# Kernel optimization log

Measured on AMD Instinct MI355X. Metric: run time of the kernel, lower is better.

Reference implementation:

```python
import jax, jax.numpy as jnp
import numpy as np

N, M, D = 256, 1024, 512


def setup_inputs() -> dict:
    key = jax.random.key(0)
    ks = jax.random.split(key, 12)
    s = 1.0 / np.sqrt(D)
    return {
        "q": jax.random.normal(ks[0], (N, D), jnp.float32),
        "k": jax.random.normal(ks[1], (M, D), jnp.float32),
        "v": jax.random.normal(ks[2], (M, D), jnp.float32),
        "mask": jax.random.randint(ks[3], (N, M), 0, 2, jnp.int32),
        "WQ": jax.random.normal(ks[4], (D, D), jnp.float32) * s,
        "bQ": jax.random.normal(ks[5], (D,), jnp.float32) * s,
        "WK": jax.random.normal(ks[6], (D, D), jnp.float32) * s,
        "bK": jax.random.normal(ks[7], (D,), jnp.float32) * s,
        "WV": jax.random.normal(ks[8], (D, D), jnp.float32) * s,
        "bV": jax.random.normal(ks[9], (D,), jnp.float32) * s,
        "Ww": jax.random.normal(ks[10], (1, D), jnp.float32) * s,
        "bw": jax.random.normal(ks[11], (1,), jnp.float32) * s,
    }


def reference(q, k, v, mask, WQ, bQ, WK, bK, WV, bV, Ww, bw):
    # Linear projections (torch Linear: x @ W.T + b)
    qp = q @ WQ.T + bQ            # [N, D]
    kp = k @ WK.T + bK            # [M, D]
    vp = v @ WV.T + bV            # [M, D]
    # Additive (Bahdanau) scores: tanh(q_n + k_m) . w  -> [N, M]
    t = jnp.tanh(qp[:, None, :] + kp[None, :, :])   # [N, M, D]
    score = jnp.einsum("nmd,d->nm", t, Ww[0]) + bw[0]
    score = jnp.where(mask == 1, score, jnp.float32(-1e6))
    w = jax.nn.softmax(score, axis=1)               # softmax over keys (dim 1)
    context = jnp.einsum("nm,md->nd", w, vp)        # weighted sum over keys
    return context
```

## Files before the change

### kernel.cpp

```cpp
#include <hip/hip_runtime.h>

#define NQ 256
#define MK 1024
#define DD 512
#define CSC 2.8853900817779268f

__global__ __launch_bounds__(256) void proj_all(
    const float* __restrict__ q, const float* __restrict__ k, const float* __restrict__ v,
    const float* __restrict__ WQ, const float* __restrict__ bQ,
    const float* __restrict__ WK, const float* __restrict__ bK,
    const float* __restrict__ WV, const float* __restrict__ bV,
    float* __restrict__ qs, float* __restrict__ kts, float* __restrict__ vp)
{
    int t = blockIdx.x;
    const float *X, *W, *b;
    int mode, i0, j0;
    if (t < 32)       { mode = 0; X = q; W = WQ; b = bQ; }
    else if (t < 160) { mode = 1; t -= 32;  X = k; W = WK; b = bK; }
    else              { mode = 2; t -= 160; X = v; W = WV; b = bV; }
    i0 = (t >> 3) * 64;
    j0 = (t & 7) * 64;

    __shared__ float Xs[16][68];
    __shared__ float Ws[16][68];
    const int tid = threadIdx.x;
    const int tx = tid & 15, ty = tid >> 4;
    const int si = tid & 63;
    const int sk = (tid >> 6) * 4;

    float4 xa = *(const float4*)&X[(i0 + si) * DD + sk];
    float4 wa = *(const float4*)&W[(j0 + si) * DD + sk];

    float acc[4][4] = {};
    for (int k0 = 0; k0 < DD; k0 += 16) {
        Xs[sk + 0][si] = xa.x; Xs[sk + 1][si] = xa.y; Xs[sk + 2][si] = xa.z; Xs[sk + 3][si] = xa.w;
        Ws[sk + 0][si] = wa.x; Ws[sk + 1][si] = wa.y; Ws[sk + 2][si] = wa.z; Ws[sk + 3][si] = wa.w;
        __syncthreads();
        if (k0 + 16 < DD) {
            xa = *(const float4*)&X[(i0 + si) * DD + k0 + 16 + sk];
            wa = *(const float4*)&W[(j0 + si) * DD + k0 + 16 + sk];
        }
#pragma unroll
        for (int kk = 0; kk < 16; ++kk) {
            float4 a4 = *(const float4*)&Xs[kk][ty * 4];
            float4 w4 = *(const float4*)&Ws[kk][tx * 4];
            float av[4] = {a4.x, a4.y, a4.z, a4.w};
            float wv[4] = {w4.x, w4.y, w4.z, w4.w};
#pragma unroll
            for (int r = 0; r < 4; ++r)
#pragma unroll
                for (int c = 0; c < 4; ++c)
                    acc[r][c] = fmaf(av[r], wv[c], acc[r][c]);
        }
        __syncthreads();
    }

    float4 bias = *(const float4*)&b[j0 + tx * 4];
    float bv[4] = {bias.x, bias.y, bias.z, bias.w};

    if (mode == 1) {
#pragma unroll
        for (int c = 0; c < 4; ++c) {
            float4 o;
            o.x = (acc[0][c] + bv[c]) * CSC;
            o.y = (acc[1][c] + bv[c]) * CSC;
            o.z = (acc[2][c] + bv[c]) * CSC;
            o.w = (acc[3][c] + bv[c]) * CSC;
            *(float4*)&kts[(j0 + tx * 4 + c) * MK + i0 + ty * 4] = o;
        }
    } else {
        float* dst = (mode == 0) ? qs : vp;
        const float sc = (mode == 0) ? CSC : 1.0f;
#pragma unroll
        for (int r = 0; r < 4; ++r) {
            float4 o;
            o.x = (acc[r][0] + bv[0]) * sc;
            o.y = (acc[r][1] + bv[1]) * sc;
            o.z = (acc[r][2] + bv[2]) * sc;
            o.w = (acc[r][3] + bv[3]) * sc;
            *(float4*)&dst[(i0 + ty * 4 + r) * DD + j0 + tx * 4] = o;
        }
    }
}

#define SNG 4

__global__ __launch_bounds__(256) void score_v2(
    const float* __restrict__ qs, const float* __restrict__ kts,
    const float* __restrict__ Ww, const float* __restrict__ bw,
    const int* __restrict__ mask, float* __restrict__ S)
{
    const int lane = threadIdx.x & 63;
    const int wave = threadIdx.x >> 6;
    const int m = blockIdx.x * 64 + lane;
    const int n0 = blockIdx.y * SNG;
    const int d0 = wave * 128;

    __shared__ float part[4][SNG][64];

    float acc[SNG] = {0.f, 0.f, 0.f, 0.f};
    float kv[8], kvn[8];
#pragma unroll
    for (int j = 0; j < 8; ++j) kv[j] = kts[(d0 + j) * MK + m];

    for (int d = d0; d < d0 + 128; d += 8) {
        if (d + 8 < d0 + 128) {
#pragma unroll
            for (int j = 0; j < 8; ++j) kvn[j] = kts[(d + 8 + j) * MK + m];
        }
#pragma unroll
        for (int j = 0; j < 8; ++j) {
            const float ww = Ww[d + j];
#pragma unroll
            for (int n = 0; n < SNG; ++n) {
                float x = qs[(n0 + n) * DD + d + j] + kv[j];
                float e = __builtin_amdgcn_exp2f(x);
                float r = __builtin_amdgcn_rcpf(e + 1.0f);
                acc[n] = fmaf(ww, r, acc[n]);
            }
        }
#pragma unroll
        for (int j = 0; j < 8; ++j) kv[j] = kvn[j];
    }

#pragma unroll
    for (int n = 0; n < SNG; ++n) part[wave][n][lane] = acc[n];
    __syncthreads();

    if (wave == 0) {
        float4 wa = *(const float4*)&Ww[lane * 8];
        float4 wb = *(const float4*)&Ww[lane * 8 + 4];
        float s = wa.x + wa.y + wa.z + wa.w + wb.x + wb.y + wb.z + wb.w;
        for (int o = 32; o > 0; o >>= 1) s += __shfl_xor(s, o, 64);
        const float cst = s + bw[0];
#pragma unroll
        for (int n = 0; n < SNG; ++n) {
            float p = part[0][n][lane] + part[1][n][lane]
                    + part[2][n][lane] + part[3][n][lane];
            float sc = fmaf(-2.0f, p, cst);
            sc = (mask[(n0 + n) * MK + m] == 1) ? sc : -1e6f;
            S[(n0 + n) * MK + m] = sc;
        }
    }
}

__global__ __launch_bounds__(256) void softmax_kernel(float* __restrict__ S)
{
    const int n = blockIdx.x;
    const int t = threadIdx.x;
    const int lane = t & 63, wave = t >> 6;
    __shared__ float red[4];

    float v[4];
    float mx = -3.4e38f;
#pragma unroll
    for (int i = 0; i < 4; ++i) {
        v[i] = S[n * MK + t + i * 256];
        mx = fmaxf(mx, v[i]);
    }
    for (int o = 32; o > 0; o >>= 1) mx = fmaxf(mx, __shfl_xor(mx, o, 64));
    if (lane == 0) red[wave] = mx;
    __syncthreads();
    mx = fmaxf(fmaxf(red[0], red[1]), fmaxf(red[2], red[3]));
    __syncthreads();

    float sum = 0.f;
#pragma unroll
    for (int i = 0; i < 4; ++i) {
        v[i] = __builtin_amdgcn_exp2f((v[i] - mx) * 1.4426950408889634f);
        sum += v[i];
    }
    for (int o = 32; o > 0; o >>= 1) sum += __shfl_xor(sum, o, 64);
    if (lane == 0) red[wave] = sum;
    __syncthreads();
    sum = red[0] + red[1] + red[2] + red[3];

    const float inv = __builtin_amdgcn_rcpf(sum);
#pragma unroll
    for (int i = 0; i < 4; ++i) S[n * MK + t + i * 256] = v[i] * inv;
}

#define CNG 8
#define CMC 256

__global__ __launch_bounds__(512) void context_v2(const float* __restrict__ S,
                                                  const float* __restrict__ vp,
                                                  float* __restrict__ out)
{
    __shared__ float ws[CMC][12];
    const int t = threadIdx.x;
    const int n0 = blockIdx.x * CNG;
    const int m0 = blockIdx.y * CMC;

#pragma unroll
    for (int p = 0; p < 4; ++p) {
        int e = t + p * 512;
        int m = e & 255, n = e >> 8;
        ws[m][n] = S[(n0 + n) * MK + m0 + m];
    }
    __syncthreads();

    float acc[CNG] = {};
    for (int m = 0; m < CMC; ++m) {
        float vv = vp[(m0 + m) * DD + t];
        float4 w0 = *(const float4*)&ws[m][0];
        float4 w4 = *(const float4*)&ws[m][4];
        acc[0] = fmaf(w0.x, vv, acc[0]);
        acc[1] = fmaf(w0.y, vv, acc[1]);
        acc[2] = fmaf(w0.z, vv, acc[2]);
        acc[3] = fmaf(w0.w, vv, acc[3]);
        acc[4] = fmaf(w4.x, vv, acc[4]);
        acc[5] = fmaf(w4.y, vv, acc[5]);
        acc[6] = fmaf(w4.z, vv, acc[6]);
        acc[7] = fmaf(w4.w, vv, acc[7]);
    }
#pragma unroll
    for (int n = 0; n < CNG; ++n) atomicAdd(&out[(n0 + n) * DD + t], acc[n]);
}

extern "C" void kernel_launch(void* const* d_in, const int* in_sizes, int n_in,
                              void* d_out, int out_size, void* d_ws, size_t ws_size,
                              hipStream_t stream)
{
    const float* q    = (const float*)d_in[0];
    const float* k    = (const float*)d_in[1];
    const float* v    = (const float*)d_in[2];
    const int*   mask = (const int*)  d_in[3];
    const float* WQ   = (const float*)d_in[4];
    const float* bQ   = (const float*)d_in[5];
    const float* WK   = (const float*)d_in[6];
    const float* bK   = (const float*)d_in[7];
    const float* WV   = (const float*)d_in[8];
    const float* bV   = (const float*)d_in[9];
    const float* Ww   = (const float*)d_in[10];
    const float* bw   = (const float*)d_in[11];
    float* out = (float*)d_out;

    float* qs  = (float*)d_ws;
    float* kts = qs + NQ * DD;
    float* vp  = kts + DD * MK;
    float* S   = vp + MK * DD;

    hipMemsetAsync(d_out, 0, (size_t)NQ * DD * sizeof(float), stream);

    proj_all<<<288, 256, 0, stream>>>(q, k, v, WQ, bQ, WK, bK, WV, bV, qs, kts, vp);

    score_v2<<<dim3(MK / 64, NQ / SNG), 256, 0, stream>>>(qs, kts, Ww, bw, mask, S);

    softmax_kernel<<<NQ, 256, 0, stream>>>(S);

    context_v2<<<dim3(NQ / CNG, MK / CMC), dim3(512), 0, stream>>>(S, vp, out);
}
```

Measured before the change: 166.5 us.

## Split-K projection GEMM with atomic accumulation and vectorize score-kernel loads

The projection kernel now splits the 512-long reduction into two halves, doubling the block count to 576 so more compute units stay busy. Partial sums are combined with per-element atomicAdd, which needs an extra memset of the workspace, and the bias is added only by the first half. The score kernel also loads q and Ww eight at a time as float4 into registers instead of one scalar per use. In exchange, the projections pay for scalar atomic traffic instead of float4 stores, plus an extra memset launch.

```diff
diff --git a/kernel.cpp b/kernel.cpp
--- a/kernel.cpp
+++ b/kernel.cpp
@@ -12,7 +12,9 @@
     const float* __restrict__ WV, const float* __restrict__ bV,
     float* __restrict__ qs, float* __restrict__ kts, float* __restrict__ vp)
 {
-    int t = blockIdx.x;
+    const int u = blockIdx.x;
+    const int kb = u & 1;
+    int t = u >> 1;
     const float *X, *W, *b;
     int mode, i0, j0;
     if (t < 32)       { mode = 0; X = q; W = WQ; b = bQ; }
@@ -20,6 +22,7 @@
     else              { mode = 2; t -= 160; X = v; W = WV; b = bV; }
     i0 = (t >> 3) * 64;
     j0 = (t & 7) * 64;
+    const int kbase = kb * 256;
 
     __shared__ float Xs[16][68];
     __shared__ float Ws[16][68];
@@ -28,15 +31,15 @@
     const int si = tid & 63;
     const int sk = (tid >> 6) * 4;
 
-    float4 xa = *(const float4*)&X[(i0 + si) * DD + sk];
-    float4 wa = *(const float4*)&W[(j0 + si) * DD + sk];
+    float4 xa = *(const float4*)&X[(i0 + si) * DD + kbase + sk];
+    float4 wa = *(const float4*)&W[(j0 + si) * DD + kbase + sk];
 
     float acc[4][4] = {};
-    for (int k0 = 0; k0 < DD; k0 += 16) {
+    for (int k0 = kbase; k0 < kbase + 256; k0 += 16) {
         Xs[sk + 0][si] = xa.x; Xs[sk + 1][si] = xa.y; Xs[sk + 2][si] = xa.z; Xs[sk + 3][si] = xa.w;
         Ws[sk + 0][si] = wa.x; Ws[sk + 1][si] = wa.y; Ws[sk + 2][si] = wa.z; Ws[sk + 3][si] = wa.w;
         __syncthreads();
-        if (k0 + 16 < DD) {
+        if (k0 + 16 < kbase + 256) {
             xa = *(const float4*)&X[(i0 + si) * DD + k0 + 16 + sk];
             wa = *(const float4*)&W[(j0 + si) * DD + k0 + 16 + sk];
         }
@@ -56,30 +59,25 @@
     }
 
     float4 bias = *(const float4*)&b[j0 + tx * 4];
-    float bv[4] = {bias.x, bias.y, bias.z, bias.w};
+    const float bs = (kb == 0) ? 1.0f : 0.0f;
+    float bv[4] = {bias.x * bs, bias.y * bs, bias.z * bs, bias.w * bs};
 
     if (mode == 1) {
 #pragma unroll
-        for (int c = 0; c < 4; ++c) {
-            float4 o;
-            o.x = (acc[0][c] + bv[c]) * CSC;
-            o.y = (acc[1][c] + bv[c]) * CSC;
-            o.z = (acc[2][c] + bv[c]) * CSC;
-            o.w = (acc[3][c] + bv[c]) * CSC;
-            *(float4*)&kts[(j0 + tx * 4 + c) * MK + i0 + ty * 4] = o;
-        }
+        for (int c = 0; c < 4; ++c)
+#pragma unroll
+            for (int r = 0; r < 4; ++r)
+                atomicAdd(&kts[(j0 + tx * 4 + c) * MK + i0 + ty * 4 + r],
+                          (acc[r][c] + bv[c]) * CSC);
     } else {
         float* dst = (mode == 0) ? qs : vp;
         const float sc = (mode == 0) ? CSC : 1.0f;
 #pragma unroll
-        for (int r = 0; r < 4; ++r) {
-            float4 o;
-            o.x = (acc[r][0] + bv[0]) * sc;
-            o.y = (acc[r][1] + bv[1]) * sc;
-            o.z = (acc[r][2] + bv[2]) * sc;
-            o.w = (acc[r][3] + bv[3]) * sc;
-            *(float4*)&dst[(i0 + ty * 4 + r) * DD + j0 + tx * 4] = o;
-        }
+        for (int r = 0; r < 4; ++r)
+#pragma unroll
+            for (int c = 0; c < 4; ++c)
+                atomicAdd(&dst[(i0 + ty * 4 + r) * DD + j0 + tx * 4 + c],
+                          (acc[r][c] + bv[c]) * sc);
     }
 }
 
@@ -103,20 +101,34 @@
 #pragma unroll
     for (int j = 0; j < 8; ++j) kv[j] = kts[(d0 + j) * MK + m];
 
-    for (int d = d0; d < d0 + 128; d += 8) {
-        if (d + 8 < d0 + 128) {
+    for (int c = 0; c < 16; ++c) {
+        const int d = d0 + c * 8;
+        float wwv[8], qv[SNG][8];
+        {
+            float4 w0 = *(const float4*)&Ww[d];
+            float4 w1 = *(const float4*)&Ww[d + 4];
+            wwv[0] = w0.x; wwv[1] = w0.y; wwv[2] = w0.z; wwv[3] = w0.w;
+            wwv[4] = w1.x; wwv[5] = w1.y; wwv[6] = w1.z; wwv[7] = w1.w;
+#pragma unroll
+            for (int n = 0; n < SNG; ++n) {
+                float4 a = *(const float4*)&qs[(n0 + n) * DD + d];
+                float4 bq = *(const float4*)&qs[(n0 + n) * DD + d + 4];
+                qv[n][0] = a.x;  qv[n][1] = a.y;  qv[n][2] = a.z;  qv[n][3] = a.w;
+                qv[n][4] = bq.x; qv[n][5] = bq.y; qv[n][6] = bq.z; qv[n][7] = bq.w;
+            }
+        }
+        if (c + 1 < 16) {
 #pragma unroll
             for (int j = 0; j < 8; ++j) kvn[j] = kts[(d + 8 + j) * MK + m];
         }
 #pragma unroll
         for (int j = 0; j < 8; ++j) {
-            const float ww = Ww[d + j];
 #pragma unroll
             for (int n = 0; n < SNG; ++n) {
-                float x = qs[(n0 + n) * DD + d + j] + kv[j];
+                float x = qv[n][j] + kv[j];
                 float e = __builtin_amdgcn_exp2f(x);
                 float r = __builtin_amdgcn_rcpf(e + 1.0f);
-                acc[n] = fmaf(ww, r, acc[n]);
+                acc[n] = fmaf(wwv[j], r, acc[n]);
             }
         }
 #pragma unroll
@@ -241,9 +253,10 @@
     float* vp  = kts + DD * MK;
     float* S   = vp + MK * DD;
 
+    hipMemsetAsync(d_ws, 0, (size_t)(NQ * DD + DD * MK + MK * DD) * sizeof(float), stream);
     hipMemsetAsync(d_out, 0, (size_t)NQ * DD * sizeof(float), stream);
 
-    proj_all<<<288, 256, 0, stream>>>(q, k, v, WQ, bQ, WK, bK, WV, bV, qs, kts, vp);
+    proj_all<<<576, 256, 0, stream>>>(q, k, v, WQ, bQ, WK, bK, WV, bV, qs, kts, vp);
 
     score_v2<<<dim3(MK / 64, NQ / SNG), 256, 0, stream>>>(qs, kts, Ww, bw, mask, S);
 
```

Result: slower. 182.7 us (+9.7%).
